# Optimization experiments

Measured on AMD Instinct MI355X. Metric: run time of the kernel, lower is better.

## Reference

```python
import jax, jax.numpy as jnp
import numpy as np

EPS = 1e-8
SAMPLE = 4          # minimal_sample_size for homography
BATCH = 1024        # batch_size: hypotheses per iteration
MAX_ITER = 10       # max_iter
MAX_LO = 5          # max_lo_iters
INL_TH = 2.0        # inl_th (on squared transfer error, as in kornia)
CONF = 0.99         # confidence
SOFT_INL_TH = 3.0   # kornia find_homography_dlt_iterated default
DLT_ITERS = 5       # kornia iterated-DLT default n_iter
N_PTS = 4096


def to_homog(p):
    return jnp.concatenate([p, jnp.ones_like(p[..., :1])], axis=-1)


def transform_points(T, p):
    # T: (B,3,3), p: (B,N,2)
    out = jnp.einsum('bij,bnj->bni', T, to_homog(p))
    z = out[..., 2:3]
    zi = jnp.where(jnp.abs(z) > EPS, 1.0 / z, 1.0)
    return out[..., :2] * zi


def normalize_points(p):
    # Hartley normalization: zero mean, mean distance sqrt(2)
    mean = p.mean(axis=1, keepdims=True)                       # (B,1,2)
    scale = jnp.linalg.norm(p - mean, axis=-1).mean(axis=-1)    # (B,)
    s = jnp.asarray(np.sqrt(2.0), p.dtype) / (scale + EPS)
    z = jnp.zeros_like(s)
    o = jnp.ones_like(s)
    T = jnp.stack([s, z, -s * mean[:, 0, 0],
                   z, s, -s * mean[:, 0, 1],
                   z, z, o], axis=-1).reshape(-1, 3, 3)
    return transform_points(T, p), T


def find_homography_dlt(p1, p2, w):
    # p1, p2: (B,N,2); w: (B,N) -> (B,3,3)
    p1n, T1 = normalize_points(p1)
    p2n, T2 = normalize_points(p2)
    x1, y1 = p1n[..., 0], p1n[..., 1]
    x2, y2 = p2n[..., 0], p2n[..., 1]
    o = jnp.ones_like(x1)
    z = jnp.zeros_like(x1)
    ax = jnp.stack([z, z, z, -x1, -y1, -o, y2 * x1, y2 * y1, y2], axis=-1)
    ay = jnp.stack([x1, y1, o, z, z, z, -x2 * x1, -x2 * y1, -x2], axis=-1)
    A = jnp.concatenate([ax, ay], axis=1)           # (B,2N,9); row order irrelevant for A^T W A
    wr = jnp.concatenate([w, w], axis=1)            # weight paired to each row
    AtWA = jnp.einsum('bni,bn,bnj->bij', A, wr, A)  # (B,9,9) symmetric PSD
    _, evecs = jnp.linalg.eigh(AtWA)
    H = evecs[..., :, 0].reshape(-1, 3, 3)          # smallest eigenvector == last right-singular vec
    H = jnp.linalg.inv(T2) @ H @ T1
    return H / (H[..., 2:3, 2:3] + EPS)


def oneway_transfer_error(kp1, kp2, models, squared=True):
    # kp1, kp2: (N,2); models: (B,3,3) -> (B,N)
    out = jnp.einsum('bij,nj->bni', models, to_homog(kp1))
    z = out[..., 2:3]
    zi = jnp.where(jnp.abs(z) > EPS, 1.0 / z, 1.0)
    proj = out[..., :2] * zi
    err = jnp.sum((proj - kp2[None]) ** 2, axis=-1)
    return err if squared else jnp.sqrt(err + EPS)


def find_homography_dlt_iterated(p1, p2, w):
    # iteratively reweighted DLT; mask keeps zero-weight (outlier) rows at zero,
    # equivalent to kornia's hard selection of inlier rows before polishing
    mask = (w > 0).astype(w.dtype)
    H = find_homography_dlt(p1, p2, w)
    for _ in range(DLT_ITERS - 1):
        err = oneway_transfer_error(p1[0], p2[0], H, squared=False)
        w = mask * jnp.exp(-err / (2.0 * SOFT_INL_TH ** 2))
        H = find_homography_dlt(p1, p2, w)
    return H


def sample_is_valid_for_homography(p1, p2):
    # orientation consistency of all point triplets (sign of triple product)
    idx = jnp.array([[0, 1, 2], [0, 1, 3], [0, 2, 3], [1, 2, 3]])
    s1 = jnp.sign(jnp.linalg.det(to_homog(p1)[:, idx]))
    s2 = jnp.sign(jnp.linalg.det(to_homog(p2)[:, idx]))
    return jnp.all(s1 == s2, axis=1)


def ransac_forward(kp1, kp2):
    N = kp1.shape[0]
    dtype = kp1.dtype
    keys = jax.random.split(jax.random.key(42), MAX_ITER)

    def verify(models):
        err = oneway_transfer_error(kp1, kp2, models)
        inl = err <= INL_TH
        return inl, inl.astype(dtype).sum(axis=1)

    def polish_step(carry, _):
        model, inliers, score, active = carry
        w = inliers.astype(dtype)[None]
        model_lo = find_homography_dlt_iterated(kp1[None], kp2[None], w)
        inl_lo, score_lo = verify(model_lo)
        better = active & (score_lo[0] > score)  # 'break' on first non-improvement
        model = jnp.where(better, model_lo[0], model)
        inliers = jnp.where(better, inl_lo[0], inliers)
        score = jnp.where(better, score_lo[0], score)
        return (model, inliers, score, better), None

    def step(carry, xs):
        best_model, best_inl, best_score, done = carry
        key, i = xs
        # minimal sampler: topk over uniform noise == random 4-subset per hypothesis
        rand = jax.random.uniform(key, (BATCH, N), dtype)
        _, idxs = jax.lax.top_k(rand, SAMPLE)
        k1s, k2s = kp1[idxs], kp2[idxs]              # (BATCH,4,2)
        valid = sample_is_valid_for_homography(k1s, k2s)
        models = find_homography_dlt(k1s, k2s, jnp.ones((BATCH, SAMPLE), dtype))
        diag_ok = jnp.abs(jnp.diagonal(models, axis1=1, axis2=2)).min(axis=1) > 1e-4
        inl_all, scores = verify(models)
        scores = jnp.where(valid & diag_ok, scores, -1.0)  # masking == removal for argmax
        bi = jnp.argmax(scores)
        model, inliers, score = models[bi], inl_all[bi], scores[bi]
        improve = (~done) & (score > best_score)
        (model_p, inl_p, score_p, _), _ = jax.lax.scan(
            polish_step, (model, inliers, score, improve), None, length=MAX_LO)
        best_model = jnp.where(improve, model_p, best_model)
        best_inl = jnp.where(improve, inl_p, best_inl)
        best_score = jnp.where(improve, score_p, best_score)
        # early stopping criterion (device-side instead of host .item())
        ratio = jnp.floor(best_score) / N
        q = jnp.clip(1.0 - ratio ** SAMPLE, 1e-12, 1.0 - 1e-12)
        max_samp = jnp.where(best_score >= N, 1.0,
                             jnp.log(1.0 - CONF) / jnp.log(q))
        done = done | (improve & (((i + 1) * BATCH) >= jnp.floor(max_samp)))
        return (best_model, best_inl, best_score, done), None

    init = (jnp.zeros((3, 3), dtype), jnp.zeros((N,), bool),
            jnp.asarray(float(SAMPLE), dtype), jnp.asarray(False))
    (best_model, best_inl, _, _), _ = jax.lax.scan(
        step, init, (keys, jnp.arange(MAX_ITER)))
    return best_model, best_inl


def setup_inputs() -> dict:
    key = jax.random.key(0)
    k1, k2, k3, k4 = jax.random.split(key, 4)
    kp1 = jax.random.uniform(k1, (N_PTS, 2), jnp.float32) * 1024.0
    Ht = jnp.array([[0.9, 0.1, 20.0], [-0.05, 1.05, -10.0], [1e-4, -1e-4, 1.0]], jnp.float32)
    ph = to_homog(kp1) @ Ht.T
    p2 = ph[:, :2] / ph[:, 2:3]
    noise = jax.random.normal(k2, (N_PTS, 2), jnp.float32) * 0.3
    outliers = jax.random.uniform(k3, (N_PTS, 2), jnp.float32) * 1024.0
    is_out = jax.random.uniform(k4, (N_PTS, 1)) < 0.3
    kp2 = jnp.where(is_out, outliers, p2 + noise)
    return {"kp1": kp1, "kp2": kp2}


def reference(kp1, kp2):
    return ransac_forward(kp1, kp2)
```

## Files before the change

kernel.cpp:

```cpp
#include <hip/hip_runtime.h>
#include <cstdint>

#define JAX_PARTITIONABLE 1

#define NPTS   4096
#define NBATCH 1024
#define NIT    10

__host__ __device__ inline uint32_t rotl32(uint32_t v, uint32_t r){ return (v<<r)|(v>>(32u-r)); }

__host__ __device__ inline void tf2x32(uint32_t k0,uint32_t k1,uint32_t x0,uint32_t x1,
                                       uint32_t&o0,uint32_t&o1){
  uint32_t ks2 = k0 ^ k1 ^ 0x1BD11BDAu;
  x0 += k0; x1 += k1;
  x0+=x1; x1=rotl32(x1,13); x1^=x0;
  x0+=x1; x1=rotl32(x1,15); x1^=x0;
  x0+=x1; x1=rotl32(x1,26); x1^=x0;
  x0+=x1; x1=rotl32(x1, 6); x1^=x0;
  x0+=k1; x1+=ks2+1u;
  x0+=x1; x1=rotl32(x1,17); x1^=x0;
  x0+=x1; x1=rotl32(x1,29); x1^=x0;
  x0+=x1; x1=rotl32(x1,16); x1^=x0;
  x0+=x1; x1=rotl32(x1,24); x1^=x0;
  x0+=ks2; x1+=k0+2u;
  x0+=x1; x1=rotl32(x1,13); x1^=x0;
  x0+=x1; x1=rotl32(x1,15); x1^=x0;
  x0+=x1; x1=rotl32(x1,26); x1^=x0;
  x0+=x1; x1=rotl32(x1, 6); x1^=x0;
  x0+=k0; x1+=k1+3u;
  x0+=x1; x1=rotl32(x1,17); x1^=x0;
  x0+=x1; x1=rotl32(x1,29); x1^=x0;
  x0+=x1; x1=rotl32(x1,16); x1^=x0;
  x0+=x1; x1=rotl32(x1,24); x1^=x0;
  x0+=k1; x1+=ks2+4u;
  x0+=x1; x1=rotl32(x1,13); x1^=x0;
  x0+=x1; x1=rotl32(x1,15); x1^=x0;
  x0+=x1; x1=rotl32(x1,26); x1^=x0;
  x0+=x1; x1=rotl32(x1, 6); x1^=x0;
  x0+=ks2; x1+=k0+5u;
  o0=x0; o1=x1;
}

__device__ inline float errsq_f(const float H[9], float x, float y, float kx, float ky){
  float z  = H[6]*x + H[7]*y + H[8];
  float zi = (fabsf(z) > 1e-8f) ? (1.0f/z) : 1.0f;
  float px = (H[0]*x + H[1]*y + H[2])*zi;
  float py = (H[3]*x + H[4]*y + H[5])*zi;
  float dx = px - kx, dy = py - ky;
  return dx*dx + dy*dy;
}

__device__ inline void denorm_h(const double h[9], double s1, double m1x, double m1y,
                                double s2, double m2x, double m2y, float out[9]){
  double G[3][3];
  #pragma unroll
  for(int r=0;r<3;r++){
    double h0=h[3*r], h1=h[3*r+1], h2=h[3*r+2];
    G[r][0] = h0*s1;
    G[r][1] = h1*s1;
    G[r][2] = -s1*m1x*h0 - s1*m1y*h1 + h2;
// ... 11 lines not shown
  for(int r=0;r<3;r++)
    #pragma unroll
    for(int c=0;c<3;c++)
      out[3*r+c] = (float)(Hm[r][c]*invd);
}

__device__ inline double det3c(double ax,double ay, double bx,double by, double cx,double cy){
  return ax*(by-cy) - bx*(ay-cy) + cx*(ay-by);
}

__device__ inline void h4pt(const double P[4][2], double M[3][3]){
  double c0 = det3c(P[3][0],P[3][1], P[1][0],P[1][1], P[2][0],P[2][1]);
  double c1 = det3c(P[0][0],P[0][1], P[3][0],P[3][1], P[2][0],P[2][1]);
  double c2 = det3c(P[0][0],P[0][1], P[1][0],P[1][1], P[3][0],P[3][1]);
  M[0][0]=c0*P[0][0]; M[0][1]=c1*P[1][0]; M[0][2]=c2*P[2][0];
  M[1][0]=c0*P[0][1]; M[1][1]=c1*P[1][1]; M[1][2]=c2*P[2][1];
  M[2][0]=c0;         M[2][1]=c1;         M[2][2]=c2;
}

__device__ inline void adj3(const double M[3][3], double A[3][3]){
  A[0][0]=M[1][1]*M[2][2]-M[1][2]*M[2][1];
  A[0][1]=M[0][2]*M[2][1]-M[0][1]*M[2][2];
  A[0][2]=M[0][1]*M[1][2]-M[0][2]*M[1][1];
  A[1][0]=M[1][2]*M[2][0]-M[1][0]*M[2][2];
  A[1][1]=M[0][0]*M[2][2]-M[0][2]*M[2][0];
  A[1][2]=M[0][2]*M[1][0]-M[0][0]*M[1][2];
  A[2][0]=M[1][0]*M[2][1]-M[1][1]*M[2][0];
  A[2][1]=M[0][1]*M[2][0]-M[0][0]*M[2][1];
  A[2][2]=M[0][0]*M[1][1]-M[0][1]*M[1][0];
}

__device__ inline void chol3(const double A[3][3], double L[3][3], double r[3]){
  double d0 = A[0][0]; if(d0<1e-280) d0=1e-280;
  double l00 = sqrt(d0); double q0 = 1.0/l00;
  double l10 = A[1][0]*q0, l20 = A[2][0]*q0;
  double d1 = A[1][1]-l10*l10; if(d1<1e-280) d1=1e-280;
  double l11 = sqrt(d1); double q1=1.0/l11;
  double l21 = (A[2][1]-l20*l10)*q1;
  double d2 = A[2][2]-l20*l20-l21*l21; if(d2<1e-280) d2=1e-280;
  double l22 = sqrt(d2); double q2=1.0/l22;
  L[0][0]=l00; L[1][0]=l10; L[1][1]=l11; L[2][0]=l20; L[2][1]=l21; L[2][2]=l22;
  r[0]=q0; r[1]=q1; r[2]=q2;
}
__device__ inline void csolve3(const double L[3][3], const double r[3],
                               const double b[3], double x[3]){
  double y0=b[0]*r[0];
  double y1=(b[1]-L[1][0]*y0)*r[1];
  double y2=(b[2]-L[2][0]*y0-L[2][1]*y1)*r[2];
  x[2]=y2*r[2];
  x[1]=(y1-L[2][1]*x[2])*r[1];
  x[0]=(y0-L[1][0]*x[1]-L[2][0]*x[2])*r[0];
}

__global__ __launch_bounds__(1024) void k_init(const float* __restrict__ kp1,
                                               const float* __restrict__ kp2,
                                               float* stateF, float* nrm,
                                               float* best_inl, float* p1n, float* p2n){
  __shared__ double red[1024];
  const int t = threadIdx.x;
  auto blk_reduce = [&](double v)->double{
    red[t]=v; __syncthreads();
    for(int off=512; off>=1; off>>=1){ if(t<off) red[t]+=red[t+off]; __syncthreads(); }
    double rr = red[0]; __syncthreads(); return rr;
  };
  double sx1=0, sy1=0, sx2=0, sy2=0;
  #pragma unroll
  for(int q=0;q<4;q++){
    int p = t + 1024*q;
    sx1 += (double)kp1[2*p];   sy1 += (double)kp1[2*p+1];
    sx2 += (double)kp2[2*p];   sy2 += (double)kp2[2*p+1];
  }
  double m1x = blk_reduce(sx1)/(double)NPTS;
  double m1y = blk_reduce(sy1)/(double)NPTS;
  double m2x = blk_reduce(sx2)/(double)NPTS;
  double m2y = blk_reduce(sy2)/(double)NPTS;
  double a1=0, a2=0;
  #pragma unroll
  for(int q=0;q<4;q++){
    int p = t + 1024*q;
    double dx1=(double)kp1[2*p]-m1x, dy1=(double)kp1[2*p+1]-m1y;
    double dx2=(double)kp2[2*p]-m2x, dy2=(double)kp2[2*p+1]-m2y;
    a1 += sqrt(dx1*dx1+dy1*dy1);
    a2 += sqrt(dx2*dx2+dy2*dy2);
  }
  double sc1 = blk_reduce(a1)/(double)NPTS;
  double sc2 = blk_reduce(a2)/(double)NPTS;
  double s1 = 1.4142135623730951/(sc1+1e-8);
  double s2 = 1.4142135623730951/(sc2+1e-8);
  if(t==0){
    nrm[0]=(float)s1; nrm[1]=(float)m1x; nrm[2]=(float)m1y;
    nrm[3]=(float)s2; nrm[4]=(float)m2x; nrm[5]=(float)m2y;
    stateF[0]=4.0f;
    stateF[1]=0.0f;
    for(int j=0;j<9;j++) stateF[2+j]=0.0f;
  }
  #pragma unroll
  for(int q=0;q<4;q++){
    int p = t + 1024*q;
    p1n[2*p]   = (float)(s1*((double)kp1[2*p]  -m1x));
    p1n[2*p+1] = (float)(s1*((double)kp1[2*p+1]-m1y));
    p2n[2*p]   = (float)(s2*((double)kp2[2*p]  -m2x));
    p2n[2*p+1] = (float)(s2*((double)kp2[2*p+1]-m2y));
    best_inl[p] = 0.0f;
  }
}

__device__ inline void ins4(uint64_t b[4], uint64_t k){
  if(k > b[0]){ b[3]=b[2]; b[2]=b[1]; b[1]=b[0]; b[0]=k; }
  else if(k > b[1]){ b[3]=b[2]; b[2]=b[1]; b[1]=k; }
  else if(k > b[2]){ b[3]=b[2]; b[2]=k; }
  else if(k > b[3]){ b[3]=k; }
}

__global__ __launch_bounds__(256) void k_sample_score(const float* stateF,
                                                uint32_t key0, uint32_t key1,
                                                const float* __restrict__ kp1,
                                                const float* __restrict__ kp2,
                                                float* __restrict__ models,
                                                float* __restrict__ scores){
  if(stateF[1] != 0.0f) return;
  const int r = blockIdx.x;
  const int t = threadIdx.x;
  __shared__ uint64_t ls[256][4];
  __shared__ float sH[9];
  __shared__ int   sFlag;
  __shared__ int   redi[4];
  uint64_t b[4] = {0ull,0ull,0ull,0ull};
  #pragma unroll
  for(int j=0;j<16;j++){
    int c = t*16 + j;
    uint32_t f = (uint32_t)(r*NPTS + c);
    uint32_t a0,a1; uint32_t bits;
#if JAX_PARTITIONABLE
    tf2x32(key0,key1, 0u, f, a0,a1);
    bits = a0 ^ a1;
#else
    const uint32_t HALF = (uint32_t)(NBATCH*NPTS/2);
    if(f < HALF){ tf2x32(key0,key1, f, f+HALF, a0,a1); bits = a0; }
    else        { tf2x32(key0,key1, f-HALF, f, a0,a1); bits = a1; }
#endif
    uint64_t v = (uint64_t)((bits>>9) + 1u);
    uint64_t key = (v<<12) | (uint64_t)(4095 - c);
    ins4(b, key);
  }
  ls[t][0]=b[0]; ls[t][1]=b[1]; ls[t][2]=b[2]; ls[t][3]=b[3];
  __syncthreads();
  for(int off=128; off>=1; off>>=1){
    if(t < off){
      uint64_t o0=ls[t+off][0], o1=ls[t+off][1], o2=ls[t+off][2], o3=ls[t+off][3];
      ins4(b,o0); ins4(b,o1); ins4(b,o2); ins4(b,o3);
      ls[t][0]=b[0]; ls[t][1]=b[1]; ls[t][2]=b[2]; ls[t][3]=b[3];
    }
    __syncthreads();
  }
  if(t==0){
    double P1[4][2], P2[4][2];
    #pragma unroll
    for(int k=0;k<4;k++){
      int id = 4095 - (int)(b[k] & 0xFFFull);
      P1[k][0]=(double)kp1[2*id]; P1[k][1]=(double)kp1[2*id+1];
      P2[k][0]=(double)kp2[2*id]; P2[k][1]=(double)kp2[2*id+1];
    }
    const int TRI[4][3] = {{0,1,2},{0,1,3},{0,2,3},{1,2,3}};
    bool valid = true;
    #pragma unroll
    for(int tq=0;tq<4;tq++){
      const int i0=TRI[tq][0], i1=TRI[tq][1], i2=TRI[tq][2];
      double d1 = det3c(P1[i0][0],P1[i0][1], P1[i1][0],P1[i1][1], P1[i2][0],P1[i2][1]);
      double d2 = det3c(P2[i0][0],P2[i0][1], P2[i1][0],P2[i1][1], P2[i2][0],P2[i2][1]);
      int s1 = (d1>0.0)-(d1<0.0), s2 = (d2>0.0)-(d2<0.0);
      if(s1 != s2) valid = false;
    }
    double MA[3][3], MB[3][3], AJ[3][3], H[3][3];
    h4pt(P1, MA); h4pt(P2, MB);
    adj3(MA, AJ);
    #pragma unroll
    for(int i=0;i<3;i++)
      #pragma unroll
      for(int j=0;j<3;j++)
        H[i][j] = MB[i][0]*AJ[0][j] + MB[i][1]*AJ[1][j] + MB[i][2]*AJ[2][j];
    double n2=0.0;
    #pragma unroll
    for(int i=0;i<3;i++)
      #pragma unroll
      for(int j=0;j<3;j++) n2 += H[i][j]*H[i][j];
    double invn = 1.0/sqrt(n2);
    double invd = 1.0/(H[2][2]*invn + 1e-8);
    float Hf[9];
    #pragma unroll
    for(int i=0;i<3;i++)
      #pragma unroll
      for(int j=0;j<3;j++) Hf[3*i+j] = (float)(H[i][j]*invn*invd);
    bool diag_ok = (fminf(fminf(fabsf(Hf[0]),fabsf(Hf[4])),fabsf(Hf[8])) > 1e-4f);
    #pragma unroll
    for(int j=0;j<9;j++){ models[r*9+j]=Hf[j]; sH[j]=Hf[j]; }
    sFlag = (valid && diag_ok) ? 1 : 0;
  }
  __syncthreads();
  float H[9];
  #pragma unroll
  for(int j=0;j<9;j++) H[j]=sH[j];
  int cnt=0;
  #pragma unroll
  for(int j=0;j<16;j++){
    int p = t + 256*j;
    float e = errsq_f(H, kp1[2*p], kp1[2*p+1], kp2[2*p], kp2[2*p+1]);
    cnt += (e <= 2.0f) ? 1 : 0;
  }
  #pragma unroll
  for(int off=32; off>=1; off>>=1) cnt += __shfl_down(cnt, off, 64);
  if((t&63)==0) redi[t>>6]=cnt;
  __syncthreads();
  if(t==0) scores[r] = sFlag ? (float)(redi[0]+redi[1]+redi[2]+redi[3]) : -1.0f;
}

__global__ __launch_bounds__(512) void k_polish(float* stateF, const float* nrm,
                                                const float* __restrict__ scores,
                                                const float* __restrict__ models,
                                                const float* __restrict__ kp1,
                                                const float* __restrict__ kp2,
                                                const float* __restrict__ p1n,
                                                const float* __restrict__ p2n,
                                                float* __restrict__ best_inl,
                                                int iter){
  if(stateF[1] != 0.0f) return;
  const int t = threadIdx.x;
  const int lane = t & 63, wv = t >> 6;
  __shared__ float  p2b[512][28];
  __shared__ double p3[16][25];
  __shared__ double sMd[24];
  __shared__ uint64_t redu[8];
  __shared__ int   redi[8];
  __shared__ float sScore;
  __shared__ float sModel[9];
  __shared__ float curHn[9];
  __shared__ float curH[9];
  __shared__ unsigned char inlb[2][NPTS];

  {
    float sA = scores[t], sB = scores[t+512];
    uint64_t kA = ((uint64_t)(uint32_t)(int)(sA + 2.0f) << 12) | (uint64_t)(1023 - t);
    uint64_t kB = ((uint64_t)(uint32_t)(int)(sB + 2.0f) << 12) | (uint64_t)(1023 - (t+512));
    uint64_t k = (kA >= kB) ? kA : kB;
    #pragma unroll
    for(int off=32; off>=1; off>>=1){
      uint64_t o = __shfl_down(k, off, 64);
      if(o > k) k = o;
    }
    if(lane==0) redu[wv]=k;
// ... 41 lines not shown
  int cur = 0;
  float score = selScore;
  bool active = true;
  float wreg[8];

  const double ns1=(double)nrm[0], nm1x=(double)nrm[1], nm1y=(double)nrm[2];
  const double ns2=(double)nrm[3], nm2x=(double)nrm[4], nm2y=(double)nrm[5];
  const float s2f  = nrm[3];
  const float epsn = 1e-8f*s2f*s2f;
  const float wk   = 1.0f/(18.0f*s2f);

  auto DLT = [&](bool denorm_now){
    float part[24];
    #pragma unroll
    for(int k=0;k<24;k++) part[k]=0.0f;
    #pragma unroll
    for(int q=0;q<8;q++){
      float w = wreg[q];
      float x=X1[q], y=Y1[q], x2=X2[q], y2=Y2[q];
      float wx = w*x, wy = w*y;
      float m0=wx*x, m1=wx*y, m2=wy*y;
      float s3 = x2*x2 + y2*y2;
      part[0]+=m0; part[1]+=m1; part[2]+=m2; part[3]+=wx; part[4]+=wy; part[5]+=w;
      part[6]+=x2*m0; part[7]+=x2*m1; part[8]+=x2*m2; part[9]+=x2*wx; part[10]+=x2*wy; part[11]+=x2*w;
      part[12]+=y2*m0; part[13]+=y2*m1; part[14]+=y2*m2; part[15]+=y2*wx; part[16]+=y2*wy; part[17]+=y2*w;
      part[18]+=s3*m0; part[19]+=s3*m1; part[20]+=s3*m2; part[21]+=s3*wx; part[22]+=s3*wy; part[23]+=s3*w;
    }
    float4* rowp = reinterpret_cast<float4*>(&p2b[t][0]);
    rowp[0]=make_float4(part[0],part[1],part[2],part[3]);
    rowp[1]=make_float4(part[4],part[5],part[6],part[7]);
    rowp[2]=make_float4(part[8],part[9],part[10],part[11]);
    rowp[3]=make_float4(part[12],part[13],part[14],part[15]);
    rowp[4]=make_float4(part[16],part[17],part[18],part[19]);
    rowp[5]=make_float4(part[20],part[21],part[22],part[23]);
    __syncthreads();
    if(t<96){
      int qd = t%6, seg = t/6;
      double a0=0,a1=0,a2=0,a3=0;
      #pragma unroll
      for(int i=0;i<32;i++){
        float4 v = *reinterpret_cast<const float4*>(&p2b[seg*32+i][qd*4]);
        a0+=(double)v.x; a1+=(double)v.y; a2+=(double)v.z; a3+=(double)v.w;
      }
      p3[seg][qd*4+0]=a0; p3[seg][qd*4+1]=a1; p3[seg][qd*4+2]=a2; p3[seg][qd*4+3]=a3;
    }
    __syncthreads();
    if(t<24){
      double a=0.0;
      #pragma unroll
      for(int s=0;s<16;s++) a += p3[s][t];
      sMd[t]=a;
    }
    __syncthreads();
    if(t==0){
      double A0[3][3],A1[3][3],A2[3][3],A3[3][3];
      auto unpackd=[&](const double* s, double M[3][3]){
        M[0][0]=s[0]; M[0][1]=s[1]; M[0][2]=s[3];
        M[1][0]=s[1]; M[1][1]=s[2]; M[1][2]=s[4];
        M[2][0]=s[3]; M[2][1]=s[4]; M[2][2]=s[5];
      };
      unpackd(&sMd[0],A0); unpackd(&sMd[6],A1); unpackd(&sMd[12],A2); unpackd(&sMd[18],A3);

      double L0[3][3], q0[3];
      chol3(A0, L0, q0);
      double T1[3][3], T2[3][3];
      #pragma unroll
      for(int c=0;c<3;c++){
        double col[3]={A1[0][c],A1[1][c],A1[2][c]}, x[3];
        csolve3(L0,q0,col,x);
        T1[0][c]=x[0]; T1[1][c]=x[1]; T1[2][c]=x[2];
      }
      #pragma unroll
      for(int c=0;c<3;c++){
        double col[3]={A2[0][c],A2[1][c],A2[2][c]}, x[3];
        csolve3(L0,q0,col,x);
        T2[0][c]=x[0]; T2[1][c]=x[1]; T2[2][c]=x[2];
      }
      double Sc[3][3];
      #pragma unroll
      for(int i=0;i<3;i++)
        #pragma unroll
        for(int j=0;j<3;j++){
          double s = A3[i][j];
          #pragma unroll
          for(int k=0;k<3;k++) s -= A1[i][k]*T1[k][j] + A2[i][k]*T2[k][j];
          Sc[i][j]=s;
        }
      double Ls[3][3], qs[3];
      chol3(Sc, Ls, qs);

      double v[9];
      #pragma unroll
      for(int i=0;i<9;i++) v[i]=1.0;
      #pragma unroll
      for(int itn=0; itn<2; itn++){
        double a[3]={v[0],v[1],v[2]}, bb[3]={v[3],v[4],v[5]}, cc[3]={v[6],v[7],v[8]};
        double w1[3],w2[3];
        csolve3(L0,q0,a,w1); csolve3(L0,q0,bb,w2);
        double rhs[3];
        #pragma unroll
        for(int j=0;j<3;j++)
          rhs[j] = cc[j] + T1[0][j]*a[0]+T1[1][j]*a[1]+T1[2][j]*a[2]
                         + T2[0][j]*bb[0]+T2[1][j]*bb[1]+T2[2][j]*bb[2];
        double rr[3];
        csolve3(Ls,qs,rhs,rr);
        #pragma unroll
        for(int i=0;i<3;i++){
          v[i]   = w1[i] + T1[i][0]*rr[0]+T1[i][1]*rr[1]+T1[i][2]*rr[2];
          v[3+i] = w2[i] + T2[i][0]*rr[0]+T2[i][1]*rr[1]+T2[i][2]*rr[2];
          v[6+i] = rr[i];
        }
        if(itn==0){
          double mx=0.0;
          #pragma unroll
          for(int i=0;i<9;i++){ double aa=fabs(v[i]); if(aa>mx) mx=aa; }
          double sc = 1.0/(mx + 1e-300);
          #pragma unroll
          for(int i=0;i<9;i++) v[i]*=sc;
        }
      }
      double n2=0.0;
      #pragma unroll
      for(int i=0;i<9;i++) n2 += v[i]*v[i];
      double invn = 1.0/sqrt(n2);
      #pragma unroll
      for(int i=0;i<9;i++) v[i]*=invn;
      #pragma unroll
      for(int j=0;j<9;j++) curHn[j]=(float)v[j];
      if(denorm_now) denorm_h(v, ns1,nm1x,nm1y, ns2,nm2x,nm2y, curH);
    }
    __syncthreads();
  };

  for(int lo=0; lo<5; lo++){
    #pragma unroll
    for(int q=0;q<8;q++){ int p=t+512*q; wreg[q] = inlb[cur][p] ? 1.0f : 0.0f; }
    DLT(false);
    for(int itp=0; itp<4; itp++){
      float Hn[9];
      #pragma unroll
      for(int j=0;j<9;j++) Hn[j]=curHn[j];
      #pragma unroll
      for(int q=0;q<8;q++){
        int p=t+512*q;
        float zn = Hn[6]*X1[q] + Hn[7]*Y1[q] + Hn[8];
        float zi = 1.0f/zn;
        float dx = (Hn[0]*X1[q] + Hn[1]*Y1[q] + Hn[2])*zi - X2[q];
        float dy = (Hn[3]*X1[q] + Hn[4]*Y1[q] + Hn[5])*zi - Y2[q];
        float err = sqrtf(dx*dx + dy*dy + epsn);
        wreg[q] = inlb[cur][p] ? __expf(-err*wk) : 0.0f;
      }
      DLT(itp==3);
    }
    float scoreLo;
    {
      float H[9];
      #pragma unroll
      for(int j=0;j<9;j++) H[j]=curH[j];
      int c=0;
      #pragma unroll
      for(int q=0;q<8;q++){
        int p=t+512*q;
        float e = errsq_f(H, U1[q],V1[q],U2[q],V2[q]);
        unsigned char bb = (e <= 2.0f) ? 1 : 0;
        inlb[cur^1][p] = bb;
        c += bb;
      }
      #pragma unroll
      for(int off=32; off>=1; off>>=1) c += __shfl_down(c, off, 64);
      if(lane==0) redi[wv]=c;
      __syncthreads();
      if(t==0){
        int s=0;
        #pragma unroll
        for(int w8=0;w8<8;w8++) s += redi[w8];
        sScore=(float)s;
      }
      __syncthreads();
      scoreLo = sScore;
    }
    bool better = active && (scoreLo > score);
    if(better){
      if(t<9) sModel[t]=curH[t];
      cur ^= 1;
      score = scoreLo;
    }
    active = better;
    __syncthreads();
    if(!active) break;
  }

  if(t<9) stateF[2+t] = sModel[t];
  #pragma unroll
  for(int q=0;q<8;q++){ int p=t+512*q; best_inl[p] = inlb[cur][p] ? 1.0f : 0.0f; }
  if(t==0){
    stateF[0] = score;
    float ratio = floorf(score) / 4096.0f;
    float r2 = ratio*ratio, r4 = r2*r2;
    float q  = 1.0f - r4;
    q = fminf(fmaxf(q, 1e-12f), (float)(1.0 - 1e-12));
    float max_samp = (score >= 4096.0f) ? 1.0f : (logf(0.01f)/logf(q));
    stateF[1] = (((float)((iter+1)*NBATCH)) >= floorf(max_samp)) ? 1.0f : 0.0f;
  }
}

__global__ __launch_bounds__(1024) void k_out(const float* stateF, const float* best_inl,
                                              float* __restrict__ out, int out_size){
  const int t = threadIdx.x;
  if(t<9 && t<out_size) out[t] = stateF[2+t];
  #pragma unroll
  for(int q=0;q<4;q++){
    int p = t + 1024*q, o = 9 + p;
    if(o < out_size) out[o] = best_inl[p];
  }
}

static void host_keys(uint32_t* K0h, uint32_t* K1h){
#if JAX_PARTITIONABLE
  for(int i=0;i<10;i++){ uint32_t a,b; tf2x32(0u,42u,0u,(uint32_t)i,a,b); K0h[i]=a; K1h[i]=b; }
#else
  uint32_t arr[20];
  for(int j=0;j<10;j++){ uint32_t a,b; tf2x32(0u,42u,(uint32_t)j,(uint32_t)(j+10),a,b); arr[j]=a; arr[j+10]=b; }
  for(int i=0;i<10;i++){ K0h[i]=arr[2*i]; K1h[i]=arr[2*i+1]; }
#endif
}

extern "C" void kernel_launch(void* const* d_in, const int* in_sizes, int n_in,
                              void* d_out, int out_size, void* d_ws, size_t ws_size,
                              hipStream_t stream) {
  const float* kp1 = (const float*)d_in[0];
  const float* kp2 = (const float*)d_in[1];
  float* out = (float*)d_out;
  float* ws  = (float*)d_ws;

  float* stateF   = ws + 0;
  float* nrm      = ws + 16;
  float* best_inl = ws + 32;
  float* p1n      = ws + 4128;
  float* p2n      = ws + 12320;
  float* scores   = ws + 20512;
  float* models   = ws + 21536;

  uint32_t K0h[10], K1h[10];
  host_keys(K0h, K1h);

  k_init<<<1, 1024, 0, stream>>>(kp1, kp2, stateF, nrm, best_inl, p1n, p2n);
  for(int i=0;i<NIT;i++){
    k_sample_score<<<NBATCH, 256, 0, stream>>>(stateF, K0h[i], K1h[i], kp1, kp2, models, scores);
    k_polish<<<1, 512, 0, stream>>>(stateF, nrm, scores, models, kp1, kp2, p1n, p2n, best_inl, i);
  }
  k_out<<<1, 1024, 0, stream>>>(stateF, best_inl, out, out_size);
}
```

Measured before the change: 126.4 us.

## Fuse all RANSAC stages into one persistent cooperative kernel with grid barriers

Replaces the chain of init, per-iteration sample/score and polish kernel launches with a single cooperative kernel of 256 blocks, each scoring 4 hypotheses per iteration. A custom atomic grid barrier separates the scoring phase from the polish phase, and block 0 handles init, polish and output. The intent is to remove the cost of about 22 kernel launches and the serialization gaps between them. In exchange, scoring uses 4x fewer blocks with more work each, polish runs on 256 threads instead of 512, and the spinning grid barrier adds its own overhead. A fallback to the old multi-kernel path remains if cooperative launch is unavailable.

```diff
diff --git a/kernel.cpp b/kernel.cpp
--- a/kernel.cpp
+++ b/kernel.cpp
@@ -1,11 +1,13 @@
 #include <hip/hip_runtime.h>
 #include <cstdint>
-
-#define JAX_PARTITIONABLE 1
 
 #define NPTS   4096
 #define NBATCH 1024
 #define NIT    10
+#define CNBLK  256
+#define CTPB   256
+#define RPB    4
+#define PPT    16
 
 __host__ __device__ inline uint32_t rotl32(uint32_t v, uint32_t r){ return (v<<r)|(v>>(32u-r)); }
 
@@ -123,6 +125,128 @@
   x[0]=(y0-L[1][0]*x[1]-L[2][0]*x[2])*r[0];
 }
 
+__device__ inline void ins4(uint64_t b[4], uint64_t k){
+  if(k > b[0]){ b[3]=b[2]; b[2]=b[1]; b[1]=b[0]; b[0]=k; }
+  else if(k > b[1]){ b[3]=b[2]; b[2]=b[1]; b[1]=k; }
+  else if(k > b[2]){ b[3]=b[2]; b[2]=k; }
+  else if(k > b[3]){ b[3]=k; }
+}
+
+__device__ inline void solve24(const double* sMd, float curHn[9], float curH[9],
+                               bool dnorm, double ns1,double nm1x,double nm1y,
+                               double ns2,double nm2x,double nm2y){
+  double A0[3][3],A1[3][3],A2[3][3],A3[3][3];
+  auto unpackd=[&](const double* s, double M[3][3]){
+    M[0][0]=s[0]; M[0][1]=s[1]; M[0][2]=s[3];
+    M[1][0]=s[1]; M[1][1]=s[2]; M[1][2]=s[4];
+    M[2][0]=s[3]; M[2][1]=s[4]; M[2][2]=s[5];
+  };
+  unpackd(sMd+0,A0); unpackd(sMd+6,A1); unpackd(sMd+12,A2); unpackd(sMd+18,A3);
+
+  double L0[3][3], q0[3];
+  chol3(A0, L0, q0);
+  double T1[3][3], T2[3][3];
+  #pragma unroll
+  for(int c=0;c<3;c++){
+    double col[3]={A1[0][c],A1[1][c],A1[2][c]}, x[3];
+    csolve3(L0,q0,col,x);
+    T1[0][c]=x[0]; T1[1][c]=x[1]; T1[2][c]=x[2];
+  }
+  #pragma unroll
+  for(int c=0;c<3;c++){
+    double col[3]={A2[0][c],A2[1][c],A2[2][c]}, x[3];
+    csolve3(L0,q0,col,x);
+    T2[0][c]=x[0]; T2[1][c]=x[1]; T2[2][c]=x[2];
+  }
+  double Sc[3][3];
+  #pragma unroll
+  for(int i=0;i<3;i++)
+    #pragma unroll
+    for(int j=0;j<3;j++){
+      double s = A3[i][j];
+      #pragma unroll
+      for(int k=0;k<3;k++) s -= A1[i][k]*T1[k][j] + A2[i][k]*T2[k][j];
+      Sc[i][j]=s;
+    }
+  double Ls[3][3], qs[3];
+  chol3(Sc, Ls, qs);
+
+  double v[9];
+  #pragma unroll
+  for(int i=0;i<9;i++) v[i]=1.0;
+  #pragma unroll
+  for(int itn=0; itn<2; itn++){
+    double a[3]={v[0],v[1],v[2]}, bb2[3]={v[3],v[4],v[5]}, cc[3]={v[6],v[7],v[8]};
+    double w1[3],w2[3];
+    csolve3(L0,q0,a,w1); csolve3(L0,q0,bb2,w2);
+    double rhs[3];
+    #pragma unroll
+    for(int j=0;j<3;j++)
+      rhs[j] = cc[j] + T1[0][j]*a[0]+T1[1][j]*a[1]+T1[2][j]*a[2]
+                     + T2[0][j]*bb2[0]+T2[1][j]*bb2[1]+T2[2][j]*bb2[2];
+    double rr[3];
+    csolve3(Ls,qs,rhs,rr);
+    #pragma unroll
+    for(int i=0;i<3;i++){
+      v[i]   = w1[i] + T1[i][0]*rr[0]+T1[i][1]*rr[1]+T1[i][2]*rr[2];
+      v[3+i] = w2[i] + T2[i][0]*rr[0]+T2[i][1]*rr[1]+T2[i][2]*rr[2];
+      v[6+i] = rr[i];
+    }
+    if(itn==0){
+      double mx=0.0;
+      #pragma unroll
+      for(int i=0;i<9;i++){ double aa=fabs(v[i]); if(aa>mx) mx=aa; }
+      double sc = 1.0/(mx + 1e-300);
+      #pragma unroll
+      for(int i=0;i<9;i++) v[i]*=sc;
+    }
+  }
+  double n2=0.0;
+  #pragma unroll
+  for(int i=0;i<9;i++) n2 += v[i]*v[i];
+  double invn = 1.0/sqrt(n2);
+  #pragma unroll
+  for(int i=0;i<9;i++) v[i]*=invn;
+  #pragma unroll
+  for(int j=0;j<9;j++) curHn[j]=(float)v[j];
+  if(dnorm) denorm_h(v, ns1,nm1x,nm1y, ns2,nm2x,nm2y, curH);
+}
+
+__device__ inline void model4(const double P1[4][2], const double P2[4][2],
+                              float Hf[9], int* flag){
+  const int TRI[4][3] = {{0,1,2},{0,1,3},{0,2,3},{1,2,3}};
+  bool valid = true;
+  #pragma unroll
+  for(int tq=0;tq<4;tq++){
+    const int i0=TRI[tq][0], i1=TRI[tq][1], i2=TRI[tq][2];
+    double d1 = det3c(P1[i0][0],P1[i0][1], P1[i1][0],P1[i1][1], P1[i2][0],P1[i2][1]);
+    double d2 = det3c(P2[i0][0],P2[i0][1], P2[i1][0],P2[i1][1], P2[i2][0],P2[i2][1]);
+    int s1 = (d1>0.0)-(d1<0.0), s2 = (d2>0.0)-(d2<0.0);
+    if(s1 != s2) valid = false;
+  }
+  double MA[3][3], MB[3][3], AJ[3][3], H[3][3];
+  h4pt(P1, MA); h4pt(P2, MB);
+  adj3(MA, AJ);
+  #pragma unroll
+  for(int i=0;i<3;i++)
+    #pragma unroll
+    for(int j=0;j<3;j++)
+      H[i][j] = MB[i][0]*AJ[0][j] + MB[i][1]*AJ[1][j] + MB[i][2]*AJ[2][j];
+  double n2=0.0;
+  #pragma unroll
+  for(int i=0;i<3;i++)
+    #pragma unroll
+    for(int j=0;j<3;j++) n2 += H[i][j]*H[i][j];
+  double invn = 1.0/sqrt(n2);
+  double invd = 1.0/(H[2][2]*invn + 1e-8);
+  #pragma unroll
+  for(int i=0;i<3;i++)
+    #pragma unroll
+    for(int j=0;j<3;j++) Hf[3*i+j] = (float)(H[i][j]*invn*invd);
+  bool diag_ok = (fminf(fminf(fabsf(Hf[0]),fabsf(Hf[4])),fabsf(Hf[8])) > 1e-4f);
+  *flag = (valid && diag_ok) ? 1 : 0;
+}
+
 __global__ __launch_bounds__(1024) void k_init(const float* __restrict__ kp1,
                                                const float* __restrict__ kp2,
                                                float* stateF, float* nrm,
@@ -161,8 +285,7 @@
   if(t==0){
     nrm[0]=(float)s1; nrm[1]=(float)m1x; nrm[2]=(float)m1y;
     nrm[3]=(float)s2; nrm[4]=(float)m2x; nrm[5]=(float)m2y;
-    stateF[0]=4.0f;
-    stateF[1]=0.0f;
+    stateF[0]=4.0f; stateF[1]=0.0f;
     for(int j=0;j<9;j++) stateF[2+j]=0.0f;
   }
   #pragma unroll
@@ -174,13 +297,6 @@
     p2n[2*p+1] = (float)(s2*((double)kp2[2*p+1]-m2y));
     best_inl[p] = 0.0f;
   }
-}
-
-__device__ inline void ins4(uint64_t b[4], uint64_t k){
-  if(k > b[0]){ b[3]=b[2]; b[2]=b[1]; b[1]=b[0]; b[0]=k; }
-  else if(k > b[1]){ b[3]=b[2]; b[2]=b[1]; b[1]=k; }
-  else if(k > b[2]){ b[3]=b[2]; b[2]=k; }
-  else if(k > b[3]){ b[3]=k; }
 }
 
 __global__ __launch_bounds__(256) void k_sample_score(const float* stateF,
@@ -201,15 +317,9 @@
   for(int j=0;j<16;j++){
     int c = t*16 + j;
     uint32_t f = (uint32_t)(r*NPTS + c);
-    uint32_t a0,a1; uint32_t bits;
-#if JAX_PARTITIONABLE
+    uint32_t a0,a1;
     tf2x32(key0,key1, 0u, f, a0,a1);
-    bits = a0 ^ a1;
-#else
-    const uint32_t HALF = (uint32_t)(NBATCH*NPTS/2);
-    if(f < HALF){ tf2x32(key0,key1, f, f+HALF, a0,a1); bits = a0; }
-    else        { tf2x32(key0,key1, f-HALF, f, a0,a1); bits = a1; }
-#endif
+    uint32_t bits = a0 ^ a1;
     uint64_t v = (uint64_t)((bits>>9) + 1u);
     uint64_t key = (v<<12) | (uint64_t)(4095 - c);
     ins4(b, key);
@@ -232,40 +342,11 @@
       P1[k][0]=(double)kp1[2*id]; P1[k][1]=(double)kp1[2*id+1];
       P2[k][0]=(double)kp2[2*id]; P2[k][1]=(double)kp2[2*id+1];
     }
-    const int TRI[4][3] = {{0,1,2},{0,1,3},{0,2,3},{1,2,3}};
-    bool valid = true;
-    #pragma unroll
-    for(int tq=0;tq<4;tq++){
-      const int i0=TRI[tq][0], i1=TRI[tq][1], i2=TRI[tq][2];
-      double d1 = det3c(P1[i0][0],P1[i0][1], P1[i1][0],P1[i1][1], P1[i2][0],P1[i2][1]);
-      double d2 = det3c(P2[i0][0],P2[i0][1], P2[i1][0],P2[i1][1], P2[i2][0],P2[i2][1]);
-      int s1 = (d1>0.0)-(d1<0.0), s2 = (d2>0.0)-(d2<0.0);
-      if(s1 != s2) valid = false;
-    }
-    double MA[3][3], MB[3][3], AJ[3][3], H[3][3];
-    h4pt(P1, MA); h4pt(P2, MB);
-    adj3(MA, AJ);
-    #pragma unroll
-    for(int i=0;i<3;i++)
-      #pragma unroll
-      for(int j=0;j<3;j++)
-        H[i][j] = MB[i][0]*AJ[0][j] + MB[i][1]*AJ[1][j] + MB[i][2]*AJ[2][j];
-    double n2=0.0;
-    #pragma unroll
-    for(int i=0;i<3;i++)
-      #pragma unroll
-      for(int j=0;j<3;j++) n2 += H[i][j]*H[i][j];
-    double invn = 1.0/sqrt(n2);
-    double invd = 1.0/(H[2][2]*invn + 1e-8);
-    float Hf[9];
-    #pragma unroll
-    for(int i=0;i<3;i++)
-      #pragma unroll
-      for(int j=0;j<3;j++) Hf[3*i+j] = (float)(H[i][j]*invn*invd);
-    bool diag_ok = (fminf(fminf(fabsf(Hf[0]),fabsf(Hf[4])),fabsf(Hf[8])) > 1e-4f);
+    float Hf[9]; int fl;
+    model4(P1,P2,Hf,&fl);
     #pragma unroll
     for(int j=0;j<9;j++){ models[r*9+j]=Hf[j]; sH[j]=Hf[j]; }
-    sFlag = (valid && diag_ok) ? 1 : 0;
+    sFlag = fl;
   }
   __syncthreads();
   float H[9];
@@ -413,83 +494,7 @@
       sMd[t]=a;
     }
     __syncthreads();
-    if(t==0){
-      double A0[3][3],A1[3][3],A2[3][3],A3[3][3];
-      auto unpackd=[&](const double* s, double M[3][3]){
-        M[0][0]=s[0]; M[0][1]=s[1]; M[0][2]=s[3];
-        M[1][0]=s[1]; M[1][1]=s[2]; M[1][2]=s[4];
-        M[2][0]=s[3]; M[2][1]=s[4]; M[2][2]=s[5];
-      };
-      unpackd(&sMd[0],A0); unpackd(&sMd[6],A1); unpackd(&sMd[12],A2); unpackd(&sMd[18],A3);
-
-      double L0[3][3], q0[3];
-      chol3(A0, L0, q0);
-      double T1[3][3], T2[3][3];
-      #pragma unroll
-      for(int c=0;c<3;c++){
-        double col[3]={A1[0][c],A1[1][c],A1[2][c]}, x[3];
-        csolve3(L0,q0,col,x);
-        T1[0][c]=x[0]; T1[1][c]=x[1]; T1[2][c]=x[2];
-      }
-      #pragma unroll
-      for(int c=0;c<3;c++){
-        double col[3]={A2[0][c],A2[1][c],A2[2][c]}, x[3];
-        csolve3(L0,q0,col,x);
-        T2[0][c]=x[0]; T2[1][c]=x[1]; T2[2][c]=x[2];
-      }
-      double Sc[3][3];
-      #pragma unroll
-      for(int i=0;i<3;i++)
-        #pragma unroll
-        for(int j=0;j<3;j++){
-          double s = A3[i][j];
-          #pragma unroll
-          for(int k=0;k<3;k++) s -= A1[i][k]*T1[k][j] + A2[i][k]*T2[k][j];
-          Sc[i][j]=s;
-        }
-      double Ls[3][3], qs[3];
-      chol3(Sc, Ls, qs);
-
-      double v[9];
-      #pragma unroll
-      for(int i=0;i<9;i++) v[i]=1.0;
-      #pragma unroll
-      for(int itn=0; itn<2; itn++){
-        double a[3]={v[0],v[1],v[2]}, bb[3]={v[3],v[4],v[5]}, cc[3]={v[6],v[7],v[8]};
-        double w1[3],w2[3];
-        csolve3(L0,q0,a,w1); csolve3(L0,q0,bb,w2);
-        double rhs[3];
-        #pragma unroll
-        for(int j=0;j<3;j++)
-          rhs[j] = cc[j] + T1[0][j]*a[0]+T1[1][j]*a[1]+T1[2][j]*a[2]
-                         + T2[0][j]*bb[0]+T2[1][j]*bb[1]+T2[2][j]*bb[2];
-        double rr[3];
-        csolve3(Ls,qs,rhs,rr);
-        #pragma unroll
-        for(int i=0;i<3;i++){
-          v[i]   = w1[i] + T1[i][0]*rr[0]+T1[i][1]*rr[1]+T1[i][2]*rr[2];
-          v[3+i] = w2[i] + T2[i][0]*rr[0]+T2[i][1]*rr[1]+T2[i][2]*rr[2];
-          v[6+i] = rr[i];
-        }
-        if(itn==0){
-          double mx=0.0;
-          #pragma unroll
-          for(int i=0;i<9;i++){ double aa=fabs(v[i]); if(aa>mx) mx=aa; }
-          double sc = 1.0/(mx + 1e-300);
-          #pragma unroll
-          for(int i=0;i<9;i++) v[i]*=sc;
-        }
-      }
-      double n2=0.0;
-      #pragma unroll
-      for(int i=0;i<9;i++) n2 += v[i]*v[i];
-      double invn = 1.0/sqrt(n2);
-      #pragma unroll
-      for(int i=0;i<9;i++) v[i]*=invn;
-      #pragma unroll
-      for(int j=0;j<9;j++) curHn[j]=(float)v[j];
-      if(denorm_now) denorm_h(v, ns1,nm1x,nm1y, ns2,nm2x,nm2y, curH);
-    }
+    if(t==0) solve24(sMd, curHn, curH, denorm_now, ns1,nm1x,nm1y, ns2,nm2x,nm2y);
     __syncthreads();
   };
 
@@ -576,14 +581,380 @@
   }
 }
 
-static void host_keys(uint32_t* K0h, uint32_t* K1h){
-#if JAX_PARTITIONABLE
-  for(int i=0;i<10;i++){ uint32_t a,b; tf2x32(0u,42u,0u,(uint32_t)i,a,b); K0h[i]=a; K1h[i]=b; }
-#else
-  uint32_t arr[20];
-  for(int j=0;j<10;j++){ uint32_t a,b; tf2x32(0u,42u,(uint32_t)j,(uint32_t)(j+10),a,b); arr[j]=a; arr[j+10]=b; }
-  for(int i=0;i<10;i++){ K0h[i]=arr[2*i]; K1h[i]=arr[2*i+1]; }
-#endif
+struct ShSample {
+  unsigned long long ls[CTPB][4];
+  float sH[9];
+  int   sFlag;
+  int   redi[4];
+};
+struct ShPolish {
+  float  p2b[CTPB][28];
+  double p3[16][25];
+  double sMd[24];
+  unsigned long long redu[4];
+  int    redi[4];
+  float  sScore;
+  float  sModel[9];
+  float  curHn[9];
+  float  curH[9];
+};
+struct ShInit {
+  double arr[CTPB][4];
+  double res[4];
+};
+union ShAll { ShSample s; ShPolish p; ShInit i; };
+
+__device__ inline void gridbar(uint32_t* cnt, uint32_t* gen, uint32_t nblk){
+  __threadfence();
+  __syncthreads();
+  if(threadIdx.x==0){
+    uint32_t g = __hip_atomic_load(gen, __ATOMIC_ACQUIRE, __HIP_MEMORY_SCOPE_AGENT);
+    uint32_t a = __hip_atomic_fetch_add(cnt, 1u, __ATOMIC_ACQ_REL, __HIP_MEMORY_SCOPE_AGENT);
+    if(a == nblk-1u){
+      __hip_atomic_store(cnt, 0u, __ATOMIC_RELAXED, __HIP_MEMORY_SCOPE_AGENT);
+      __hip_atomic_store(gen, g+1u, __ATOMIC_RELEASE, __HIP_MEMORY_SCOPE_AGENT);
+    }else{
+      while(__hip_atomic_load(gen, __ATOMIC_ACQUIRE, __HIP_MEMORY_SCOPE_AGENT) == g){
+        __builtin_amdgcn_s_sleep(2);
+      }
+    }
+  }
+  __syncthreads();
+  __threadfence();
+}
+
+__global__ __launch_bounds__(CTPB) void k_all(const float* __restrict__ kp1,
+                                              const float* __restrict__ kp2,
+                                              float* __restrict__ out, int out_size,
+                                              float* __restrict__ ws){
+  const int b = blockIdx.x;
+  const int t = threadIdx.x;
+  const int lane = t & 63, wv = t >> 6;
+
+  float* stateF   = ws + 0;
+  float* nrm      = ws + 16;
+  float* best_inl = ws + 32;
+  float* scores   = ws + 20512;
+  float* models   = ws + 21536;
+  uint32_t* barw  = (uint32_t*)(ws + 30752);
+
+  __shared__ ShAll sh;
+
+  if(b == 0){
+    double s0=0,s1=0,s2=0,s3=0;
+    #pragma unroll
+    for(int q=0;q<PPT;q++){
+      int p = t + CTPB*q;
+      float2 a = ((const float2*)kp1)[p];
+      float2 c = ((const float2*)kp2)[p];
+      s0 += (double)a.x; s1 += (double)a.y; s2 += (double)c.x; s3 += (double)c.y;
+      best_inl[p] = 0.0f;
+    }
+    sh.i.arr[t][0]=s0; sh.i.arr[t][1]=s1; sh.i.arr[t][2]=s2; sh.i.arr[t][3]=s3;
+    __syncthreads();
+    if(t < 4){
+      double a = 0;
+      for(int r=0;r<CTPB;r++) a += sh.i.arr[r][t];
+      sh.i.res[t] = a / (double)NPTS;
+    }
+    __syncthreads();
+    const double m1x = sh.i.res[0], m1y = sh.i.res[1];
+    const double m2x = sh.i.res[2], m2y = sh.i.res[3];
+    __syncthreads();
+    double a1=0, a2=0;
+    #pragma unroll
+    for(int q=0;q<PPT;q++){
+      int p = t + CTPB*q;
+      float2 a = ((const float2*)kp1)[p];
+      float2 c = ((const float2*)kp2)[p];
+      double dx1=(double)a.x-m1x, dy1=(double)a.y-m1y;
+      double dx2=(double)c.x-m2x, dy2=(double)c.y-m2y;
+      a1 += sqrt(dx1*dx1+dy1*dy1);
+      a2 += sqrt(dx2*dx2+dy2*dy2);
+    }
+    sh.i.arr[t][0]=a1; sh.i.arr[t][1]=a2;
+    __syncthreads();
+    if(t < 2){
+      double a=0;
+      for(int r=0;r<CTPB;r++) a += sh.i.arr[r][t];
+      sh.i.res[t] = a / (double)NPTS;
+    }
+    __syncthreads();
+    if(t==0){
+      double sc1 = sh.i.res[0], sc2 = sh.i.res[1];
+      double s1d = 1.4142135623730951/(sc1+1e-8);
+      double s2d = 1.4142135623730951/(sc2+1e-8);
+      nrm[0]=(float)s1d; nrm[1]=(float)m1x; nrm[2]=(float)m1y;
+      nrm[3]=(float)s2d; nrm[4]=(float)m2x; nrm[5]=(float)m2y;
+      stateF[0]=4.0f;
+      __hip_atomic_store(&stateF[1], 0.0f, __ATOMIC_RELEASE, __HIP_MEMORY_SCOPE_AGENT);
+      for(int j=0;j<9;j++) stateF[2+j]=0.0f;
+    }
+    __syncthreads();
+  }
+
+  for(int i=0;i<NIT;i++){
+    if(i > 0){
+      float dn = __hip_atomic_load(&stateF[1], __ATOMIC_ACQUIRE, __HIP_MEMORY_SCOPE_AGENT);
+      if(dn != 0.0f) break;
+    }
+    uint32_t key0, key1;
+    tf2x32(0u,42u,0u,(uint32_t)i,key0,key1);
+
+    for(int m=0;m<RPB;m++){
+      const int r = b*RPB + m;
+      uint64_t bb[4] = {0ull,0ull,0ull,0ull};
+      #pragma unroll
+      for(int j=0;j<16;j++){
+        int c = t*16 + j;
+        uint32_t f = (uint32_t)(r*NPTS + c);
+        uint32_t a0,a1;
+        tf2x32(key0,key1, 0u, f, a0,a1);
+        uint32_t bits = a0 ^ a1;
+        uint64_t v = (uint64_t)((bits>>9) + 1u);
+        uint64_t kk = (v<<12) | (uint64_t)(4095 - c);
+        ins4(bb, kk);
+      }
+      sh.s.ls[t][0]=bb[0]; sh.s.ls[t][1]=bb[1]; sh.s.ls[t][2]=bb[2]; sh.s.ls[t][3]=bb[3];
+      __syncthreads();
+      for(int off=128; off>=1; off>>=1){
+        if(t < off){
+          uint64_t o0=sh.s.ls[t+off][0], o1=sh.s.ls[t+off][1];
+          uint64_t o2=sh.s.ls[t+off][2], o3=sh.s.ls[t+off][3];
+          ins4(bb,o0); ins4(bb,o1); ins4(bb,o2); ins4(bb,o3);
+          sh.s.ls[t][0]=bb[0]; sh.s.ls[t][1]=bb[1]; sh.s.ls[t][2]=bb[2]; sh.s.ls[t][3]=bb[3];
+        }
+        __syncthreads();
+      }
+      if(t==0){
+        double P1[4][2], P2[4][2];
+        #pragma unroll
+        for(int k=0;k<4;k++){
+          int id = 4095 - (int)(bb[k] & 0xFFFull);
+          P1[k][0]=(double)kp1[2*id]; P1[k][1]=(double)kp1[2*id+1];
+          P2[k][0]=(double)kp2[2*id]; P2[k][1]=(double)kp2[2*id+1];
+        }
+        float Hf[9]; int fl;
+        model4(P1,P2,Hf,&fl);
+        #pragma unroll
+        for(int j=0;j<9;j++){ models[r*9+j]=Hf[j]; sh.s.sH[j]=Hf[j]; }
+        sh.s.sFlag = fl;
+      }
+      __syncthreads();
+      float H[9];
+      #pragma unroll
+      for(int j=0;j<9;j++) H[j]=sh.s.sH[j];
+      int cnt=0;
+      #pragma unroll
+      for(int j=0;j<PPT;j++){
+        int p = t + CTPB*j;
+        float2 a = ((const float2*)kp1)[p];
+        float2 c = ((const float2*)kp2)[p];
+        float e = errsq_f(H, a.x, a.y, c.x, c.y);
+        cnt += (e <= 2.0f) ? 1 : 0;
+      }
+      #pragma unroll
+      for(int off=32; off>=1; off>>=1) cnt += __shfl_down(cnt, off, 64);
+      if(lane==0) sh.s.redi[wv]=cnt;
+      __syncthreads();
+      if(t==0) scores[r] = sh.s.sFlag ?
+          (float)(sh.s.redi[0]+sh.s.redi[1]+sh.s.redi[2]+sh.s.redi[3]) : -1.0f;
+      __syncthreads();
+    }
+    gridbar(&barw[0], &barw[1], (uint32_t)gridDim.x);
+
+    if(b==0){
+      uint64_t k = 0;
+      #pragma unroll
+      for(int c4=0;c4<4;c4++){
+        int r = t + 256*c4;
+        float sv = __hip_atomic_load(&scores[r], __ATOMIC_ACQUIRE, __HIP_MEMORY_SCOPE_AGENT);
+        uint64_t key = ((uint64_t)(uint32_t)(int)(sv + 2.0f) << 12) | (uint64_t)(1023 - r);
+        if(key > k) k = key;
+      }
+      #pragma unroll
+      for(int off=32; off>=1; off>>=1){
+        uint64_t o = __shfl_down(k, off, 64);
+        if(o > k) k = o;
+      }
+      if(lane==0) sh.p.redu[wv]=k;
+      __syncthreads();
+      if(t==0){
+        uint64_t mm=sh.p.redu[0];
+        #pragma unroll
+        for(int w8=1;w8<4;w8++) if(sh.p.redu[w8]>mm) mm=sh.p.redu[w8];
+        sh.p.redu[0]=mm;
+      }
+      __syncthreads();
+      const int bi = 1023 - (int)(sh.p.redu[0] & 0xFFFull);
+      const float selScore = (float)((int)(sh.p.redu[0] >> 12)) - 2.0f;
+      const bool improve = (selScore > stateF[0]);
+
+      if(improve){
+        if(t<9) sh.p.sModel[t] =
+            __hip_atomic_load(&models[bi*9+t], __ATOMIC_ACQUIRE, __HIP_MEMORY_SCOPE_AGENT);
+        __syncthreads();
+
+        float U1[PPT],V1[PPT],U2[PPT],V2[PPT];
+        #pragma unroll
+        for(int q=0;q<PPT;q++){
+          int p = t + CTPB*q;
+          float2 a = ((const float2*)kp1)[p];
+          float2 c = ((const float2*)kp2)[p];
+          U1[q]=a.x; V1[q]=a.y; U2[q]=c.x; V2[q]=c.y;
+        }
+        const float s1f=nrm[0], m1xf=nrm[1], m1yf=nrm[2];
+        const float s2f=nrm[3], m2xf=nrm[4], m2yf=nrm[5];
+        const float tx1=-(s1f*m1xf), ty1=-(s1f*m1yf);
+        const float tx2=-(s2f*m2xf), ty2=-(s2f*m2yf);
+        const double ns1=(double)s1f, nm1x=(double)m1xf, nm1y=(double)m1yf;
+        const double ns2=(double)s2f, nm2x=(double)m2xf, nm2y=(double)m2yf;
+        const float epsn = 1e-8f*s2f*s2f;
+        const float wk   = 1.0f/(18.0f*s2f);
+
+        uint32_t cm = 0;
+        {
+          float H[9];
+          #pragma unroll
+          for(int j=0;j<9;j++) H[j]=sh.p.sModel[j];
+          #pragma unroll
+          for(int q=0;q<PPT;q++){
+            float e = errsq_f(H, U1[q],V1[q],U2[q],V2[q]);
+            cm |= (e <= 2.0f ? 1u : 0u) << q;
+          }
+        }
+
+        float score = selScore;
+        bool active = true;
+        float wreg[PPT];
+
+        auto DLT = [&](bool dnorm){
+          float part[24];
+          #pragma unroll
+          for(int kk=0;kk<24;kk++) part[kk]=0.0f;
+          #pragma unroll
+          for(int q=0;q<PPT;q++){
+            float w = wreg[q];
+            float x  = fmaf(s1f, U1[q], tx1), y  = fmaf(s1f, V1[q], ty1);
+            float x2 = fmaf(s2f, U2[q], tx2), y2 = fmaf(s2f, V2[q], ty2);
+            float wx = w*x, wy = w*y;
+            float m0=wx*x, m1=wx*y, m2=wy*y;
+            float s3 = x2*x2 + y2*y2;
+            part[0]+=m0; part[1]+=m1; part[2]+=m2; part[3]+=wx; part[4]+=wy; part[5]+=w;
+            part[6]+=x2*m0; part[7]+=x2*m1; part[8]+=x2*m2; part[9]+=x2*wx; part[10]+=x2*wy; part[11]+=x2*w;
+            part[12]+=y2*m0; part[13]+=y2*m1; part[14]+=y2*m2; part[15]+=y2*wx; part[16]+=y2*wy; part[17]+=y2*w;
+            part[18]+=s3*m0; part[19]+=s3*m1; part[20]+=s3*m2; part[21]+=s3*wx; part[22]+=s3*wy; part[23]+=s3*w;
+          }
+          float4* rowp = reinterpret_cast<float4*>(&sh.p.p2b[t][0]);
+          rowp[0]=make_float4(part[0],part[1],part[2],part[3]);
+          rowp[1]=make_float4(part[4],part[5],part[6],part[7]);
+          rowp[2]=make_float4(part[8],part[9],part[10],part[11]);
+          rowp[3]=make_float4(part[12],part[13],part[14],part[15]);
+          rowp[4]=make_float4(part[16],part[17],part[18],part[19]);
+          rowp[5]=make_float4(part[20],part[21],part[22],part[23]);
+          __syncthreads();
+          if(t<96){
+            int qd = t%6, seg = t/6;
+            double a0=0,a1=0,a2=0,a3=0;
+            #pragma unroll
+            for(int rr=0;rr<16;rr++){
+              float4 v = *reinterpret_cast<const float4*>(&sh.p.p2b[seg*16+rr][qd*4]);
+              a0+=(double)v.x; a1+=(double)v.y; a2+=(double)v.z; a3+=(double)v.w;
+            }
+            sh.p.p3[seg][qd*4+0]=a0; sh.p.p3[seg][qd*4+1]=a1;
+            sh.p.p3[seg][qd*4+2]=a2; sh.p.p3[seg][qd*4+3]=a3;
+          }
+          __syncthreads();
+          if(t<24){
+            double a=0.0;
+            #pragma unroll
+            for(int s=0;s<16;s++) a += sh.p.p3[s][t];
+            sh.p.sMd[t]=a;
+          }
+          __syncthreads();
+          if(t==0) solve24(sh.p.sMd, sh.p.curHn, sh.p.curH, dnorm,
+                           ns1,nm1x,nm1y, ns2,nm2x,nm2y);
+          __syncthreads();
+        };
+
+        for(int lo=0; lo<5; lo++){
+          #pragma unroll
+          for(int q=0;q<PPT;q++) wreg[q] = ((cm>>q)&1u) ? 1.0f : 0.0f;
+          DLT(false);
+          for(int itp=0; itp<4; itp++){
+            float Hn[9];
+            #pragma unroll
+            for(int j=0;j<9;j++) Hn[j]=sh.p.curHn[j];
+            #pragma unroll
+            for(int q=0;q<PPT;q++){
+              float x  = fmaf(s1f, U1[q], tx1), y  = fmaf(s1f, V1[q], ty1);
+              float x2 = fmaf(s2f, U2[q], tx2), y2 = fmaf(s2f, V2[q], ty2);
+              float zn = Hn[6]*x + Hn[7]*y + Hn[8];
+              float zi = 1.0f/zn;
+              float dx = (Hn[0]*x + Hn[1]*y + Hn[2])*zi - x2;
+              float dy = (Hn[3]*x + Hn[4]*y + Hn[5])*zi - y2;
+              float err = sqrtf(dx*dx + dy*dy + epsn);
+              wreg[q] = ((cm>>q)&1u) ? __expf(-err*wk) : 0.0f;
+            }
+            DLT(itp==3);
+          }
+          float H[9];
+          #pragma unroll
+          for(int j=0;j<9;j++) H[j]=sh.p.curH[j];
+          uint32_t nmv = 0;
+          #pragma unroll
+          for(int q=0;q<PPT;q++){
+            float e = errsq_f(H, U1[q],V1[q],U2[q],V2[q]);
+            nmv |= (e <= 2.0f ? 1u : 0u) << q;
+          }
+          int c = __popc(nmv);
+          #pragma unroll
+          for(int off=32; off>=1; off>>=1) c += __shfl_down(c, off, 64);
+          if(lane==0) sh.p.redi[wv]=c;
+          __syncthreads();
+          if(t==0) sh.p.sScore = (float)(sh.p.redi[0]+sh.p.redi[1]+sh.p.redi[2]+sh.p.redi[3]);
+          __syncthreads();
+          float scoreLo = sh.p.sScore;
+          bool better = active && (scoreLo > score);
+          if(better){
+            if(t<9) sh.p.sModel[t]=sh.p.curH[t];
+            cm = nmv;
+            score = scoreLo;
+          }
+          active = better;
+          __syncthreads();
+          if(!active) break;
+        }
+
+        if(t<9) stateF[2+t] = sh.p.sModel[t];
+        #pragma unroll
+        for(int q=0;q<PPT;q++){
+          int p = t + CTPB*q;
+          best_inl[p] = ((cm>>q)&1u) ? 1.0f : 0.0f;
+        }
+        if(t==0){
+          stateF[0] = score;
+          float ratio = floorf(score) / 4096.0f;
+          float r2 = ratio*ratio, r4 = r2*r2;
+          float q  = 1.0f - r4;
+          q = fminf(fmaxf(q, 1e-12f), (float)(1.0 - 1e-12));
+          float max_samp = (score >= 4096.0f) ? 1.0f : (logf(0.01f)/logf(q));
+          float dn = (((float)((i+1)*NBATCH)) >= floorf(max_samp)) ? 1.0f : 0.0f;
+          __hip_atomic_store(&stateF[1], dn, __ATOMIC_RELEASE, __HIP_MEMORY_SCOPE_AGENT);
+        }
+      }
+    }
+    gridbar(&barw[0], &barw[1], (uint32_t)gridDim.x);
+  }
+
+  if(b==0){
+    if(t<9 && t<out_size) out[t] = stateF[2+t];
+    #pragma unroll
+    for(int q=0;q<PPT;q++){
+      int p = t + CTPB*q, o = 9 + p;
+      if(o < out_size) out[o] = best_inl[p];
+    }
+  }
 }
 
 extern "C" void kernel_launch(void* const* d_in, const int* in_sizes, int n_in,
@@ -601,14 +972,33 @@
   float* p2n      = ws + 12320;
   float* scores   = ws + 20512;
   float* models   = ws + 21536;
-
-  uint32_t K0h[10], K1h[10];
-  host_keys(K0h, K1h);
-
-  k_init<<<1, 1024, 0, stream>>>(kp1, kp2, stateF, nrm, best_inl, p1n, p2n);
-  for(int i=0;i<NIT;i++){
-    k_sample_score<<<NBATCH, 256, 0, stream>>>(stateF, K0h[i], K1h[i], kp1, kp2, models, scores);
-    k_polish<<<1, 512, 0, stream>>>(stateF, nrm, scores, models, kp1, kp2, p1n, p2n, best_inl, i);
-  }
-  k_out<<<1, 1024, 0, stream>>>(stateF, best_inl, out, out_size);
-}
+  void*  barw     = (void*)(ws + 30752);
+
+  int dev = 0; (void)hipGetDevice(&dev);
+  int coop = 0;
+  (void)hipDeviceGetAttribute(&coop, hipDeviceAttributeCooperativeLaunch, dev);
+  int maxb = 0;
+  if(coop)
+    (void)hipOccupancyMaxActiveBlocksPerMultiprocessor(&maxb, k_all, CTPB, 0);
+
+  bool coop_ok = false;
+  if(coop && maxb >= 1){
+    (void)hipMemsetAsync(barw, 0, 16, stream);
+    void* args[] = { (void*)&kp1, (void*)&kp2, (void*)&out, (void*)&out_size, (void*)&ws };
+    hipError_t e = hipLaunchCooperativeKernel((void*)k_all, dim3(CNBLK), dim3(CTPB),
+                                              args, 0, stream);
+    if(e == hipSuccess) coop_ok = true;
+    else (void)hipGetLastError();
+  }
+
+  if(!coop_ok){
+    uint32_t K0h[10], K1h[10];
+    for(int i=0;i<10;i++){ uint32_t a,b; tf2x32(0u,42u,0u,(uint32_t)i,a,b); K0h[i]=a; K1h[i]=b; }
+    k_init<<<1, 1024, 0, stream>>>(kp1, kp2, stateF, nrm, best_inl, p1n, p2n);
+    for(int i=0;i<NIT;i++){
+      k_sample_score<<<NBATCH, 256, 0, stream>>>(stateF, K0h[i], K1h[i], kp1, kp2, models, scores);
+      k_polish<<<1, 512, 0, stream>>>(stateF, nrm, scores, models, kp1, kp2, p1n, p2n, best_inl, i);
+    }
+    k_out<<<1, 1024, 0, stream>>>(stateF, best_inl, out, out_size);
+  }
+}
```

Result: no change. 125.2 us (-0.9%).
